# Kernel optimization log

Measured on AMD Instinct MI355X. Metric: run time of the kernel, lower is better.

## Reference

```python
import jax, jax.numpy as jnp
import numpy as np
import math

B, S, H = 4, 1024, 768
NH, DH = 12, 64
POS = 2 * S
INIT_STD = 0.02


def rel_shift_bnij(x, klen):
    # x: [b, n, i, j] -> Transformer-XL relative shift
    b, n, i, j = x.shape
    x = x.reshape(b, n, j, i)
    x = x[:, :, 1:, :]
    x = x.reshape(b, n, i, j - 1)
    return x[:, :, :, :klen]


def setup_inputs() -> dict:
    key = jax.random.key(0)
    ks = jax.random.split(key, 10)
    hidden = jax.random.normal(ks[0], (B, S, H), dtype=jnp.float32)
    pos_emb = jax.random.normal(ks[1], (B, POS, H), dtype=jnp.float32)
    mask = (jax.random.uniform(ks[2], (B, S, S)) < 0.1).astype(jnp.float32)
    q = INIT_STD * jax.random.normal(ks[3], (H, NH, DH), dtype=jnp.float32)
    kv = INIT_STD * jax.random.normal(ks[4], (H, NH, DH), dtype=jnp.float32)
    r = INIT_STD * jax.random.normal(ks[5], (H, NH, DH), dtype=jnp.float32)
    r_r_bias = INIT_STD * jax.random.normal(ks[6], (NH, DH), dtype=jnp.float32)
    r_w_bias = INIT_STD * jax.random.normal(ks[7], (NH, DH), dtype=jnp.float32)
    w_out = INIT_STD * jax.random.normal(ks[8], (NH * DH, H), dtype=jnp.float32)
    b_out = jnp.zeros((H,), dtype=jnp.float32)
    return {"hidden": hidden, "pos_emb": pos_emb, "mask": mask,
            "q": q, "kv": kv, "r": r,
            "r_r_bias": r_r_bias, "r_w_bias": r_w_bias,
            "w_out": w_out, "b_out": b_out}


def reference(hidden, pos_emb, mask, q, kv, r, r_r_bias, r_w_bias, w_out, b_out):
    b, s, dim = hidden.shape
    d_head = q.shape[-1]
    q_head_h = jnp.einsum('bih,hnd->bind', hidden, q)
    kv_head_h = jnp.einsum('bih,hnd->bind', hidden, kv)
    k_head_r = jnp.einsum('bih,hnd->bind', pos_emb, r)
    # content and position score terms
    ac = jnp.einsum('bind,bjnd->bnij', q_head_h + r_w_bias, kv_head_h)
    bd = jnp.einsum('bind,bjnd->bnij', q_head_h + r_r_bias, k_head_r)
    bd = rel_shift_bnij(bd, klen=ac.shape[3])
    scores = (ac + bd) / math.sqrt(d_head)
    scores = scores + mask[:, None, :, :] * (-65500.0)
    alpha = jax.nn.softmax(scores, axis=-1)  # dropout is identity in eval
    res = jnp.einsum('bhmn,bnhd->bmhd', alpha, kv_head_h).reshape(b, s, dim)
    res = res @ w_out + b_out
    res = hidden + res  # graph_residual=True
    return jax.nn.gelu(res, approximate=False)
```

## Files before the change

kernel.cpp:

```cpp
#include <hip/hip_runtime.h>

typedef unsigned short u16;
typedef unsigned int u32;
typedef unsigned long long u64;
typedef __attribute__((ext_vector_type(8))) short bf8v;
typedef __attribute__((ext_vector_type(4))) float f32x4;
typedef __attribute__((ext_vector_type(4))) u32 u32x4;
typedef __attribute__((ext_vector_type(2))) __fp16 fp16x2;

#define S_   1024
#define POS_ 2048

__device__ __forceinline__ float b2f(u16 h){
  union { float f; unsigned u; } x; x.u = ((unsigned)h) << 16; return x.f;
}
__device__ __forceinline__ u16 f2b(float f){
  union { float f; unsigned u; } x; x.f = f;
  unsigned u = x.u;
  return (u16)((u + 0x7fffu + ((u >> 16) & 1u)) >> 16);
}
__device__ __forceinline__ u16 f2bt(float f){
  union { float f; unsigned u; } x; x.f = f;
  return (u16)(x.u >> 16);
}

#define GLDS16(g, l) __builtin_amdgcn_global_load_lds( \
    (const __attribute__((address_space(1))) unsigned int*)(g), \
    (__attribute__((address_space(3))) unsigned int*)(l), 16, 0, 0)

__global__ __launch_bounds__(256) void prep(const float* __restrict__ q, const float* __restrict__ kv,
                                            const float* __restrict__ r, const float* __restrict__ wo,
                                            u16* __restrict__ wqkv, u16* __restrict__ wout,
                                            const float* __restrict__ mask, u32* __restrict__ mbT,
                                            u16* __restrict__ zp,
                                            const float* __restrict__ hidden, const float* __restrict__ pos,
                                            u16* __restrict__ hb, u16* __restrict__ pb){
  int blk = blockIdx.x, tid = threadIdx.x;
  if (blk < 2304){
    __shared__ u16 t[32][33];
    int z = blk / 576, rem = blk % 576;
    const float* src; u16* dst;
    if (z == 0){ src = q;  dst = wqkv; }
    else if (z == 1){ src = kv; dst = wqkv + 768*768; }
    else if (z == 2){ src = r;  dst = wqkv + 2*768*768; }
    else { src = wo; dst = wout; }
    int gx = (rem % 24)*32, gy = (rem / 24)*32;
    int tx = tid & 31, ty = tid >> 5;
    #pragma unroll
    for (int k = 0; k < 4; ++k)
      t[ty + 8*k][tx] = f2b(src[(gy + ty + 8*k)*768 + gx + tx]);
    __syncthreads();
    #pragma unroll
    for (int k = 0; k < 4; ++k)
      dst[(gx + ty + 8*k)*768 + gy + tx] = t[tx][ty + 8*k];
  } else if (blk < 2816){
    int widx = (blk - 2304)*4 + (tid >> 6);
    int lane = tid & 63;
    int kt = widx & 15, bi = widx >> 4;
    const float* mrow = mask + (size_t)bi*32*1024 + kt*64 + lane;
    u32 m = 0;
    #pragma unroll
    for (int rr = 0; rr < 32; ++rr)
      m |= (mrow[(size_t)rr*1024] != 0.0f ? 1u : 0u) << rr;
    mbT[(size_t)widx*64 + lane] = m;
    if (blk == 2304 && tid < 8) zp[tid] = 0;
  } else {
    size_t i = ((size_t)(blk - 2816)*256 + tid)*8;
    const float* s; u16* d;
    if (i < 3145728){ s = hidden + i; d = hb + i; }
    else { s = pos + (i - 3145728); d = pb + (i - 3145728); }
    f32x4 x0 = *(const f32x4*)s, x1 = *(const f32x4*)(s + 4);
    bf8v t;
    #pragma unroll
    for (int j = 0; j < 4; ++j){ t[j] = f2b(x0[j]); t[4+j] = f2b(x1[j]); }
    *(bf8v*)d = t;
  }
}

template<int MODE>
__device__ __forceinline__ void gemm_core(const void* Av, int lda, const u16* Bt,
                                          u16* Cv, int ldc,
                                          int bm, int bn,
                                          u16 (*As)[32], u16 (*Bs)[32]){
  int tid = threadIdx.x;
  int lane = tid & 63, rg = tid >> 6;
  int quad = lane >> 4, l15 = lane & 15;
  int wm = rg >> 1, wn = rg & 1;
  int poff = (quad ^ ((l15 >> 1) & 3)) * 8;
  f32x4 acc[4][4];
  #pragma unroll
  for (int i = 0; i < 4; ++i)
    #pragma unroll
    for (int j = 0; j < 4; ++j)
      acc[i][j] = (f32x4){0.f,0.f,0.f,0.f};

  for (int kt = 0; kt < 24; ++kt){
    int k0 = kt*32;
    if (kt) __syncthreads();
    #pragma unroll
    for (int t = 0; t < 2; ++t){
      int m = (rg*2 + t)*16 + (lane >> 2);
      int g = ((lane & 3) ^ ((m >> 1) & 3)) * 8;
      GLDS16(&Bt[(size_t)(bn*128 + m)*768 + k0 + g], &Bs[m][(lane & 3)*8]);
    }
    if (MODE & 2){
      #pragma unroll
      for (int t = 0; t < 2; ++t){
        int m = (rg*2 + t)*16 + (lane >> 2);
        int g = ((lane & 3) ^ ((m >> 1) & 3)) * 8;
        GLDS16(&((const u16*)Av)[(size_t)(bm*128 + m)*lda + k0 + g], &As[m][(lane & 3)*8]);
      }
    } else {
      #pragma unroll
      for (int e = 0; e < 2; ++e){
        int v = tid + 256*e;
        int m = v >> 2, c = v & 3;
        const u32* ap = (const u32*)Av + (size_t)(bm*128 + m)*lda + k0 + c*8;
        u32x4 a0 = *(const u32x4*)ap;
        u32x4 a1 = *(const u32x4*)(ap + 4);
        u32x4 pk;
        pk[0] = (a0[0] >> 16) | (a0[1] & 0xFFFF0000u);
        pk[1] = (a0[2] >> 16) | (a0[3] & 0xFFFF0000u);
        pk[2] = (a1[0] >> 16) | (a1[1] & 0xFFFF0000u);
        pk[3] = (a1[2] >> 16) | (a1[3] & 0xFFFF0000u);
        *(u32x4*)&As[m][(c ^ ((m >> 1) & 3))*8] = pk;
      }
    }
    __syncthreads();
    bf8v af[4], bf[4];
    #pragma unroll
    for (int mt = 0; mt < 4; ++mt) af[mt] = *(const bf8v*)&As[wm*64 + mt*16 + l15][poff];
    #pragma unroll
    for (int nt = 0; nt < 4; ++nt) bf[nt] = *(const bf8v*)&Bs[wn*64 + nt*16 + l15][poff];
    #pragma unroll
    for (int mt = 0; mt < 4; ++mt)
      #pragma unroll
      for (int nt = 0; nt < 4; ++nt)
        acc[mt][nt] = __builtin_amdgcn_mfma_f32_16x16x32_bf16(af[mt], bf[nt], acc[mt][nt], 0, 0, 0);
  }

  #pragma unroll
  for (int mt = 0; mt < 4; ++mt)
    #pragma unroll
    for (int nt = 0; nt < 4; ++nt)
      #pragma unroll
      for (int reg = 0; reg < 4; ++reg){
        int grow = bm*128 + wm*64 + mt*16 + quad*4 + reg;
        int gcol = bn*128 + wn*64 + nt*16 + l15;
        Cv[(size_t)grow*ldc + gcol] = f2b(acc[mt][nt][reg]);
      }
}

__global__ __launch_bounds__(256) void gemm_proj(const void* __restrict__ A1, const void* __restrict__ A2,
                                                 const u16* __restrict__ wqkv,
                                                 u16* __restrict__ qkvh, u16* __restrict__ krh, int amode){
  __shared__ u16 As[128][32];
  __shared__ u16 Bs[128][32];
  int t = blockIdx.x;
  if (t < 384){
    if (amode) gemm_core<2>(A1, 768, wqkv, qkvh, 1536, t & 31, t >> 5, As, Bs);
    else       gemm_core<0>(A1, 768, wqkv, qkvh, 1536, t & 31, t >> 5, As, Bs);
  } else {
    t -= 384;
    if (amode) gemm_core<2>(A2, 768, wqkv + 2*768*768, krh, 768, t & 63, t >> 6, As, Bs);
    else       gemm_core<0>(A2, 768, wqkv + 2*768*768, krh, 768, t & 63, t >> 6, As, Bs);
  }
}

__global__ __launch_bounds__(256) void gemm_out(const u16* __restrict__ ctx, const u16* __restrict__ wout,
                                                float* __restrict__ out,
                                                const float* __restrict__ resid, const float* __restrict__ bias){
  __shared__ u16 As[64][32];
  __shared__ u16 Bs[64][32];
  int tid = threadIdx.x;
  int lane = tid & 63, rg = tid >> 6;
  int quad = lane >> 4, l15 = lane & 15;
  int wm = rg >> 1, wn = rg & 1;
  int bm = blockIdx.x, bn = blockIdx.y;
  f32x4 acc[2][2];
  #pragma unroll
  for (int i = 0; i < 2; ++i)
    #pragma unroll
    for (int j = 0; j < 2; ++j)
      acc[i][j] = (f32x4){0.f,0.f,0.f,0.f};

  int m = tid >> 2, c = tid & 3;
  int gsrc = (c ^ ((m >> 1) & 3)) * 8;
  int poff = (quad ^ ((l15 >> 1) & 3)) * 8;
  for (int kt = 0; kt < 24; ++kt){
    int k0 = kt*32;
    if (kt) __syncthreads();
    GLDS16(&ctx[(size_t)(bm*64 + m)*768 + k0 + gsrc], &As[m][c*8]);
    GLDS16(&wout[(size_t)(bn*64 + m)*768 + k0 + gsrc], &Bs[m][c*8]);
    __syncthreads();
    bf8v af[2], bf[2];
    #pragma unroll
    for (int mt = 0; mt < 2; ++mt) af[mt] = *(const bf8v*)&As[wm*32 + mt*16 + l15][poff];
    #pragma unroll
    for (int nt = 0; nt < 2; ++nt) bf[nt] = *(const bf8v*)&Bs[wn*32 + nt*16 + l15][poff];
    #pragma unroll
    for (int mt = 0; mt < 2; ++mt)
      #pragma unroll
      for (int nt = 0; nt < 2; ++nt)
        acc[mt][nt] = __builtin_amdgcn_mfma_f32_16x16x32_bf16(af[mt], bf[nt], acc[mt][nt], 0, 0, 0);
  }

  #pragma unroll
  for (int mt = 0; mt < 2; ++mt)
    #pragma unroll
    for (int nt = 0; nt < 2; ++nt)
      #pragma unroll
      for (int reg = 0; reg < 4; ++reg){
        int grow = bm*64 + wm*32 + mt*16 + quad*4 + reg;
        int gcol = bn*64 + wn*32 + nt*16 + l15;
        float v = acc[mt][nt][reg] + bias[gcol] + resid[(size_t)grow*768 + gcol];
        v = 0.5f * v * (1.0f + erff(v * 0.70710678118654752f));
        out[(size_t)grow*768 + gcol] = v;
      }
}

__global__ __launch_bounds__(256, 4) void attn(const u16* __restrict__ qkvh,
                                               const u16* __restrict__ krh,
                                               const u32* __restrict__ mbT,
                                               const float* __restrict__ rrb,
                                               const float* __restrict__ rwb,
                                               const u16* __restrict__ zp,
                                               u16* __restrict__ ctx){
  __shared__ u16 kvL[64][64];
  __shared__ u16 krL[96][64];
  __shared__ u16 pL[32][72];
  __shared__ float lpart[4][32];

  int tid = threadIdx.x;
  int lane = tid & 63, w = tid >> 6;
  int quad = lane >> 4, l15 = lane & 15;

  int fid = blockIdx.x;
  int xcd = fid & 7, loc = fid >> 3;
  int pair = xcd*6 + (loc >> 5);
  int i0 = (loc & 31) * 32;
  int b = pair / 12, n = pair % 12;

  const u16* kvbase = qkvh + (size_t)b*S_*1536 + 768 + n*64;
  const u16* krbase = krh + (size_t)b*POS_*768 + n*64;
  const float SC = 0.18033688f;

  bf8v qwf[2][2], qrf[2][2];
  #pragma unroll
  for (int rgi = 0; rgi < 2; ++rgi)
    #pragma unroll
    for (int c = 0; c < 2; ++c){
      int d0 = c*32 + quad*8;
      bf8v qv = *(const bf8v*)&qkvh[(size_t)(b*S_ + i0 + rgi*16 + l15)*1536 + n*64 + d0];
      f32x4 w0 = *(const f32x4*)&rwb[n*64 + d0];
      f32x4 w1 = *(const f32x4*)&rwb[n*64 + d0 + 4];
      f32x4 r0 = *(const f32x4*)&rrb[n*64 + d0];
      f32x4 r1 = *(const f32x4*)&rrb[n*64 + d0 + 4];
      bf8v qw, qr;
      #pragma unroll
      for (int j = 0; j < 4; ++j){
        float qf0 = b2f((u16)qv[j]), qf1 = b2f((u16)qv[4+j]);
        qw[j]   = f2b((qf0 + w0[j])*SC);
        qw[4+j] = f2b((qf1 + w1[j])*SC);
        qr[j]   = f2b((qf0 + r0[j])*SC);
        qr[4+j] = f2b((qf1 + r1[j])*SC);
      }
      qwf[rgi][c] = qw;
      qrf[rgi][c] = qr;
    }

  f32x4 ctxa[2];
  float l_acc[2][4];
  #pragma unroll
  for (int i = 0; i < 2; ++i){
    ctxa[i] = (f32x4){0.f,0.f,0.f,0.f};
    #pragma unroll
    for (int j = 0; j < 4; ++j) l_acc[i][j] = 0.f;
  }

  int key = w*16 + l15;
  int pvcol = (((key >> 3) + 2*quad) & 7)*8 + (key & 7);
  int cswz = ((l15 >> 2) & 3) << 3;
  const u32* mrowp = mbT + ((size_t)(b*32 + (i0 >> 5))*16)*64 + key;

  for (int kt = 0; kt < 16; ++kt){
    int k0 = kt*64;
    int j0 = k0 + S_ - i0 - 31;
    __syncthreads();
    #pragma unroll
    for (int e = 0; e < 2; ++e){
      int v = tid + 256*e;
      int k = v >> 3, s = v & 7;
      int g = (s - 2*(k >> 3)) & 7;
      GLDS16(&kvbase[(size_t)(k0 + k)*1536 + g*8], &kvL[k][s*8]);
    }
    #pragma unroll
    for (int e = 0; e < 3; ++e){
      int v = tid + 256*e;
      int jj = v >> 3, s = v & 7;
      int g = (s - 3*(jj >> 3)) & 7;
      int jg = j0 + jj;
      const u16* src = (jg < POS_) ? &krbase[(size_t)jg*768 + g*8] : zp;
      GLDS16(src, &krL[jj][s*8]);
    }
    u32 mrow = mrowp[(size_t)kt*64];
    __syncthreads();

    int rA = w*16 + l15;
    f32x4 ac0 = (f32x4){0.f,0.f,0.f,0.f}, ac1 = (f32x4){0.f,0.f,0.f,0.f};
    f32x4 b00 = (f32x4){0.f,0.f,0.f,0.f}, b01 = (f32x4){0.f,0.f,0.f,0.f};
    f32x4 b10 = (f32x4){0.f,0.f,0.f,0.f}, b11 = (f32x4){0.f,0.f,0.f,0.f};
    #pragma unroll
    for (int c = 0; c < 2; ++c){
      int p = (c*4 + quad + 2*(key >> 3)) & 7;
      bf8v bkv = *(const bf8v*)&kvL[key][p*8];
      ac0 = __builtin_amdgcn_mfma_f32_16x16x32_bf16(qwf[0][c], bkv, ac0, 0, 0, 0);
      ac1 = __builtin_amdgcn_mfma_f32_16x16x32_bf16(qwf[1][c], bkv, ac1, 0, 0, 0);
    }
    #pragma unroll
    for (int c = 0; c < 2; ++c){
      int rB = rA + 16;
      bf8v kB = *(const bf8v*)&krL[rB][((c*4 + quad + 3*(rB >> 3)) & 7)*8];
      b00 = __builtin_amdgcn_mfma_f32_16x16x32_bf16(qrf[0][c], kB, b00, 0, 0, 0);
      b11 = __builtin_amdgcn_mfma_f32_16x16x32_bf16(qrf[1][c], kB, b11, 0, 0, 0);
    }
    #pragma unroll
    for (int c = 0; c < 2; ++c){
      int rC = rA + 32;
      bf8v kC = *(const bf8v*)&krL[rC][((c*4 + quad + 3*(rC >> 3)) & 7)*8];
      b01 = __builtin_amdgcn_mfma_f32_16x16x32_bf16(qrf[0][c], kC, b01, 0, 0, 0);
    }
    #pragma unroll
    for (int c = 0; c < 2; ++c){
      bf8v kA = *(const bf8v*)&krL[rA][((c*4 + quad + 3*(rA >> 3)) & 7)*8];
      b10 = __builtin_amdgcn_mfma_f32_16x16x32_bf16(qrf[1][c], kA, b10, 0, 0, 0);
    }

    f32x4 acA[2]  = {ac0, ac1};
    f32x4 bdLo[2] = {b00, b10};
    f32x4 bdHi[2] = {b01, b11};
    #pragma unroll
    for (int rgi = 0; rgi < 2; ++rgi){
      u32 mq = mrow >> (rgi*16 + quad*4);
      u32 pk_[4];
      #pragma unroll
      for (int reg = 0; reg < 4; ++reg){
        union { fp16x2 h; u32 u; } cv;
        cv.h = __builtin_amdgcn_cvt_pkrtz(bdLo[rgi][reg], bdHi[rgi][reg]);
        pk_[reg] = cv.u;
      }
      #pragma unroll
      for (int reg = 0; reg < 4; ++reg){
        int sj = l15 + 15 - (quad*4 + reg);
        int srcl = (sj & 15) | (lane & 48);
        u32 got = (u32)__builtin_amdgcn_ds_bpermute(srcl << 2, (int)pk_[reg]);
        union { u16 s; __fp16 h; } hv;
        hv.s = (u16)(got >> (sj & 16));
        float sc = acA[rgi][reg] + (float)hv.h;
        float e = exp2f(sc);
        float p = ((mq >> reg) & 1u) ? 0.0f : e;
        l_acc[rgi][reg] += p;
        pL[rgi*16 + quad*4 + reg][key ^ (quad << 3)] = f2bt(p);
      }
    }
    __syncthreads();

    bf8v bv[2];
    #pragma unroll
    for (int c = 0; c < 2; ++c)
      #pragma unroll
      for (int j = 0; j < 8; ++j)
        bv[c][j] = (short)kvL[c*32 + quad*8 + j][pvcol];
    #pragma unroll
    for (int rgi = 0; rgi < 2; ++rgi)
      #pragma unroll
      for (int c = 0; c < 2; ++c){
        bf8v pa = *(const bf8v*)&pL[rgi*16 + l15][c*32 + ((quad*8) ^ cswz)];
        ctxa[rgi] = __builtin_amdgcn_mfma_f32_16x16x32_bf16(pa, bv[c], ctxa[rgi], 0, 0, 0);
      }
  }

  #pragma unroll
  for (int rgi = 0; rgi < 2; ++rgi)
    #pragma unroll
    for (int reg = 0; reg < 4; ++reg){
      float v = l_acc[rgi][reg];
      #pragma unroll
      for (int off = 1; off < 16; off <<= 1) v += __shfl_xor(v, off);
      l_acc[rgi][reg] = v;
    }
  if (l15 == 0){
    #pragma unroll
    for (int rgi = 0; rgi < 2; ++rgi)
      #pragma unroll
      for (int reg = 0; reg < 4; ++reg)
        lpart[w][rgi*16 + quad*4 + reg] = l_acc[rgi][reg];
  }
  __syncthreads();
  #pragma unroll
  for (int rgi = 0; rgi < 2; ++rgi)
    #pragma unroll
    for (int reg = 0; reg < 4; ++reg){
      int rloc = rgi*16 + quad*4 + reg;
      float lt = lpart[0][rloc] + lpart[1][rloc] + lpart[2][rloc] + lpart[3][rloc];
      ctx[(size_t)(b*S_ + i0 + rloc)*768 + n*64 + w*16 + l15] = f2b(ctxa[rgi][reg] / lt);
    }
}

extern "C" void kernel_launch(void* const* d_in, const int* in_sizes, int n_in,
                              void* d_out, int out_size, void* d_ws, size_t ws_size,
                              hipStream_t stream){
  (void)in_sizes; (void)n_in; (void)out_size;
  const float* hidden = (const float*)d_in[0];
  const float* pos    = (const float*)d_in[1];
  const float* maskp  = (const float*)d_in[2];
  const float* q      = (const float*)d_in[3];
  const float* kv     = (const float*)d_in[4];
  const float* r      = (const float*)d_in[5];
  const float* rrb    = (const float*)d_in[6];
  const float* rwb    = (const float*)d_in[7];
  const float* wo     = (const float*)d_in[8];
  const float* bo     = (const float*)d_in[9];
  float* out = (float*)d_out;

  u16* qkvh = (u16*)d_ws;
  u16* krh  = qkvh + (size_t)4096*1536;
  u16* wout = krh  + (size_t)8192*768;
  u16* wqkv = wout + 768*768;
  bool big = ws_size >= 49283104ull;
  u16 *hb = nullptr, *pb = nullptr, *ctx;
  u64* mbp;
  if (big){
    hb  = wqkv + (size_t)3*768*768;
    pb  = hb + (size_t)4096*768;
    ctx = hb;
    mbp = (u64*)(pb + (size_t)8192*768);
  } else {
    ctx = wqkv;
    mbp = (u64*)(wqkv + (size_t)4096*768);
  }
  u16* zp = (u16*)(mbp + 65536);

  prep<<<dim3(big ? 7424 : 2816), 256, 0, stream>>>(q, kv, r, wo, wqkv, wout,
                                                    maskp, (u32*)mbp, zp, hidden, pos, hb, pb);
  if (big) gemm_proj<<<dim3(768), 256, 0, stream>>>(hb, pb, wqkv, qkvh, krh, 2);
  else     gemm_proj<<<dim3(768), 256, 0, stream>>>(hidden, pos, wqkv, qkvh, krh, 0);
  attn<<<dim3(1536), 256, 0, stream>>>(qkvh, krh, (const u32*)mbp, rrb, rwb, zp, ctx);
  gemm_out<<<dim3(64,12), 256, 0, stream>>>(ctx, wout, out, hidden, bo);
}
```

Measured before the change: 220.3 us.

## Add 256x256-tile double-buffered projection GEMM for bf16-prestaged inputs

```diff
diff --git a/kernel.cpp b/kernel.cpp
--- a/kernel.cpp
+++ b/kernel.cpp
@@ -153,18 +153,92 @@
 
 __global__ __launch_bounds__(256) void gemm_proj(const void* __restrict__ A1, const void* __restrict__ A2,
                                                  const u16* __restrict__ wqkv,
-                                                 u16* __restrict__ qkvh, u16* __restrict__ krh, int amode){
+                                                 u16* __restrict__ qkvh, u16* __restrict__ krh){
   __shared__ u16 As[128][32];
   __shared__ u16 Bs[128][32];
   int t = blockIdx.x;
-  if (t < 384){
-    if (amode) gemm_core<2>(A1, 768, wqkv, qkvh, 1536, t & 31, t >> 5, As, Bs);
-    else       gemm_core<0>(A1, 768, wqkv, qkvh, 1536, t & 31, t >> 5, As, Bs);
-  } else {
-    t -= 384;
-    if (amode) gemm_core<2>(A2, 768, wqkv + 2*768*768, krh, 768, t & 63, t >> 6, As, Bs);
-    else       gemm_core<0>(A2, 768, wqkv + 2*768*768, krh, 768, t & 63, t >> 6, As, Bs);
-  }
+  if (t < 384) gemm_core<0>(A1, 768, wqkv, qkvh, 1536, t & 31, t >> 5, As, Bs);
+  else { t -= 384; gemm_core<0>(A2, 768, wqkv + 2*768*768, krh, 768, t & 63, t >> 6, As, Bs); }
+}
+
+__global__ __launch_bounds__(512, 2) void gemm256(const u16* __restrict__ A1, const u16* __restrict__ A2,
+                                                  const u16* __restrict__ wqkv,
+                                                  u16* __restrict__ qkvh, u16* __restrict__ krh){
+  __shared__ u16 As[2][256][64];
+  __shared__ u16 Bs[2][256][64];
+  int tid = threadIdx.x;
+  int lane = tid & 63, wid = tid >> 6;
+  int quad = lane >> 4, l15 = lane & 15;
+  int wm = wid >> 2, wn = wid & 3;
+
+  int t = blockIdx.x;
+  const u16 *Ap, *Bt; u16* Cv; int bm, bn, ldc;
+  if (t < 96){ Ap = A1; Bt = wqkv;               Cv = qkvh; bm = t & 15; bn = t >> 4; ldc = 1536; }
+  else { t -= 96; Ap = A2; Bt = wqkv + 2*768*768; Cv = krh;  bm = t & 31; bn = t >> 5; ldc = 768; }
+
+  const u16* arow = Ap + (size_t)(bm*256)*768;
+  const u16* brow = Bt + (size_t)(bn*256)*768;
+
+  f32x4 acc[8][4];
+  #pragma unroll
+  for (int i = 0; i < 8; ++i)
+    #pragma unroll
+    for (int j = 0; j < 4; ++j)
+      acc[i][j] = (f32x4){0.f,0.f,0.f,0.f};
+
+  #pragma unroll
+  for (int e = 0; e < 4; ++e){
+    int idx = tid + 512*e;
+    int m = idx >> 3, s = idx & 7;
+    int g = s ^ ((m >> 1) & 7);
+    GLDS16(&arow[(size_t)m*768 + g*8], &As[0][m][s*8]);
+    GLDS16(&brow[(size_t)m*768 + g*8], &Bs[0][m][s*8]);
+  }
+  __syncthreads();
+
+  for (int kt = 0; kt < 12; ++kt){
+    int cur = kt & 1;
+    if (kt < 11){
+      int k0 = (kt + 1)*64;
+      #pragma unroll
+      for (int e = 0; e < 4; ++e){
+        int idx = tid + 512*e;
+        int m = idx >> 3, s = idx & 7;
+        int g = s ^ ((m >> 1) & 7);
+        GLDS16(&arow[(size_t)m*768 + k0 + g*8], &As[cur ^ 1][m][s*8]);
+        GLDS16(&brow[(size_t)m*768 + k0 + g*8], &Bs[cur ^ 1][m][s*8]);
+      }
+    }
+    #pragma unroll
+    for (int kc = 0; kc < 2; ++kc){
+      bf8v bf[4];
+      #pragma unroll
+      for (int nt = 0; nt < 4; ++nt){
+        int r = wn*64 + nt*16 + l15;
+        bf[nt] = *(const bf8v*)&Bs[cur][r][(((kc*4 + quad) ^ ((r >> 1) & 7)))*8];
+      }
+      #pragma unroll
+      for (int mt = 0; mt < 8; ++mt){
+        int r = wm*128 + mt*16 + l15;
+        bf8v af = *(const bf8v*)&As[cur][r][(((kc*4 + quad) ^ ((r >> 1) & 7)))*8];
+        #pragma unroll
+        for (int nt = 0; nt < 4; ++nt)
+          acc[mt][nt] = __builtin_amdgcn_mfma_f32_16x16x32_bf16(af, bf[nt], acc[mt][nt], 0, 0, 0);
+      }
+    }
+    __syncthreads();
+  }
+
+  #pragma unroll
+  for (int mt = 0; mt < 8; ++mt)
+    #pragma unroll
+    for (int nt = 0; nt < 4; ++nt)
+      #pragma unroll
+      for (int reg = 0; reg < 4; ++reg){
+        int grow = bm*256 + wm*128 + mt*16 + quad*4 + reg;
+        int gcol = bn*256 + wn*64 + nt*16 + l15;
+        Cv[(size_t)grow*ldc + gcol] = f2b(acc[mt][nt][reg]);
+      }
 }
 
 __global__ __launch_bounds__(256) void gemm_out(const u16* __restrict__ ctx, const u16* __restrict__ wout,
@@ -443,8 +517,8 @@
 
   prep<<<dim3(big ? 7424 : 2816), 256, 0, stream>>>(q, kv, r, wo, wqkv, wout,
                                                     maskp, (u32*)mbp, zp, hidden, pos, hb, pb);
-  if (big) gemm_proj<<<dim3(768), 256, 0, stream>>>(hb, pb, wqkv, qkvh, krh, 2);
-  else     gemm_proj<<<dim3(768), 256, 0, stream>>>(hidden, pos, wqkv, qkvh, krh, 0);
+  if (big) gemm256<<<dim3(192), 512, 0, stream>>>(hb, pb, wqkv, qkvh, krh);
+  else     gemm_proj<<<dim3(768), 256, 0, stream>>>(hidden, pos, wqkv, qkvh, krh);
   attn<<<dim3(1536), 256, 0, stream>>>(qkvh, krh, (const u32*)mbp, rrb, rwb, zp, ctx);
   gemm_out<<<dim3(64,12), 256, 0, stream>>>(ctx, wout, out, hidden, bo);
 }
```

After: 221.9 us. Within noise of the previous version (+0.7%).
